# Kernel tuning notes

Measured on AMD Instinct MI355X. Metric: run time of the kernel, lower is better.

Reference implementation:

```python
import jax, jax.numpy as jnp
import numpy as np

N, E, F, H, C = 100000, 1600000, 64, 64, 40


def _agg_norm(row, col, mask, mtype, n):
    # A_tilde = A * mask (rows for 'target', cols for 'source'); fill_diag(A_tilde, 1.0)
    v = mask[row] if mtype == 'target' else mask[col]
    v = jnp.where(row == col, 0.0, v)  # diag entries replaced by fill_diag value 1
    deg = jax.ops.segment_sum(v, row, num_segments=n) + 1.0  # +1 from the filled diagonal
    d = jnp.where(deg > 0, jax.lax.rsqrt(deg), 0.0)  # D^-0.5, inf -> 0
    return d[row] * v * d[col], d * d  # off-diag edge values, diagonal values


def _spmm(row, col, vals, diag, x, n):
    # A_hat @ x with diagonal handled densely
    return jax.ops.segment_sum(vals[:, None] * x[col], row, num_segments=n) + diag[:, None] * x


def _sage(row, col, vals, diag, x, Wl, Wr, n):
    # SAGEConv(bias=False): lin_l(aggregate(A_hat, x)) + lin_r(x)
    return _spmm(row, col, vals, diag, x, n) @ Wl + x @ Wr


def setup_inputs() -> dict:
    key = jax.random.key(0)
    ks = jax.random.split(key, 16)
    g = lambda k, shape, s=0.1: jax.random.normal(k, shape, jnp.float32) * s
    return dict(
        x=g(ks[0], (N, F), 1.0),
        edge_index=jax.random.randint(ks[1], (2, E), 0, N),
        cc_mask=jax.random.randint(ks[2], (N,), 0, 2, dtype=jnp.int32),
        W1l=g(ks[3], (F, H)), W1r=g(ks[4], (F, H)),
        W2l=g(ks[5], (H, H)), W2r=g(ks[6], (H, H)),
        W3l=g(ks[7], (F, H)), W3r=g(ks[8], (F, H)),
        W4l=g(ks[9], (H, H)), W4r=g(ks[10], (H, H)),
        WX=g(ks[11], (F, H)),
        lam1=jnp.zeros((2,), jnp.float32),
        lam2=jnp.zeros((2,), jnp.float32),
        lin_W=g(ks[12], (H, C)),
        lin_b=jnp.zeros((C,), jnp.float32),
    )


def reference(x, edge_index, cc_mask, W1l, W1r, W2l, W2r, W3l, W3r, W4l, W4r, WX, lam1, lam2, lin_W, lin_b):
    n = x.shape[0]
    row, col = edge_index[1], edge_index[0]  # SparseTensor(row=ei[1], col=ei[0])
    cc = cc_mask.astype(x.dtype)
    rev = 1.0 - cc

    vl, dl = _agg_norm(row, col, cc, 'target', n)
    vll, dll = _agg_norm(row, col, cc, 'source', n)
    vh, dh = _agg_norm(row, col, rev, 'target', n)
    vhh, dhh = _agg_norm(row, col, rev, 'source', n)

    xl = jax.nn.relu(_sage(row, col, vl, dl, x, W1l, W1r, n))   # dropout = identity (eval)
    xl = _sage(row, col, vll, dll, xl, W2l, W2r, n)
    xh = jax.nn.relu(_sage(row, col, vh, dh, x, W3l, W3r, n))
    xh = _sage(row, col, vhh, dhh, xh, W4l, W4r, n)

    xm = x @ WX
    lamxl, laml = jax.nn.softmax(lam1)
    lamxh, lamh = jax.nn.softmax(lam2)
    lamx = lamxl * cc + lamxh * rev
    xf = jax.nn.relu(lamx[:, None] * xm + laml * xl + lamh * xh)
    return xf @ lin_W + lin_b
```

## Files before the change

### kernel.cpp

```cpp
#include <hip/hip_runtime.h>

#define PADF 68
#define RS_LOG 6
#define RSTRIDE 64


__global__ void k_deg(const int* __restrict__ ei, const int* __restrict__ cc,
                      unsigned long long* __restrict__ deg,
                      int* __restrict__ csr, int E, int H) {
    int t = blockIdx.x * blockDim.x + threadIdx.x;
    if (t >= H) return;
    int e0 = t, e1 = t + H;
    bool h1 = e1 < E;
    int c0 = ei[e0], r0 = ei[E + e0];
    int c1 = 0, r1 = 0;
    if (h1) { c1 = ei[e1]; r1 = ei[E + e1]; }
    bool a0 = (r0 != c0);
    bool a1 = h1 && (r1 != c1);
    int g0 = a0 ? (cc[c0] & 1) : 0;
    int g1 = a1 ? (cc[c1] & 1) : 0;
    unsigned long long old0 = 0, old1 = 0;
    if (a0) old0 = atomicAdd(&deg[r0], 0x100000000ULL + (unsigned long long)g0);
    if (a1) old1 = atomicAdd(&deg[r1], 0x100000000ULL + (unsigned long long)g1);
    if (a0) {
        int rk = (int)(old0 >> 32);
        if (rk < RSTRIDE)
            csr[(r0 << RS_LOG) + rk] = (int)((unsigned)c0 | ((unsigned)g0 << 31));
    }
    if (a1) {
        int rk = (int)(old1 >> 32);
        if (rk < RSTRIDE)
            csr[(r1 << RS_LOG) + rk] = (int)((unsigned)c1 | ((unsigned)g1 << 31));
    }
}

__global__ void k_dinv(const unsigned long long* __restrict__ deg,
                       const int* __restrict__ cc,
                       float* __restrict__ vs,
                       float* __restrict__ dll, float* __restrict__ dhh,
                       int* __restrict__ cnt, int n) {
    int i = blockIdx.x * blockDim.x + threadIdx.x;
    if (i >= n) return;
    unsigned long long d = deg[i];
    int c = (int)(d >> 32);
    int s = (int)(d & 0xffffffffULL);
    float fc = (float)c, fs = (float)s;
    float v = rsqrtf(fc + 1.0f);
    vs[i]  = cc[i] ? v : -v;
    dll[i] = rsqrtf(fs + 1.0f);
    dhh[i] = rsqrtf(fc - fs + 1.0f);
    cnt[i] = (c > RSTRIDE) ? RSTRIDE : c;
}


__device__ __forceinline__ void xreduce4(float4& a) {
    #pragma unroll
    for (int m = 16; m < 64; m <<= 1) {
        a.x += __shfl_xor(a.x, m, 64);
        a.y += __shfl_xor(a.y, m, 64);
        a.z += __shfl_xor(a.z, m, 64);
        a.w += __shfl_xor(a.w, m, 64);
    }
}

__device__ __forceinline__ void acc4(float4& a, float w, const float4& v) {
    a.x = fmaf(w, v.x, a.x); a.y = fmaf(w, v.y, a.y);
    a.z = fmaf(w, v.z, a.z); a.w = fmaf(w, v.w, a.w);
}

__device__ __forceinline__ void add4(float4& a, const float4& v) {
    a.x += v.x; a.y += v.y; a.z += v.z; a.w += v.w;
}

__global__ __launch_bounds__(256) void k_gather1(
        const int* __restrict__ cnt, const int* __restrict__ csr,
        const float* __restrict__ vs, const float* __restrict__ x,
        float* __restrict__ acc1, int n) {
    int w = (blockIdx.x * blockDim.x + threadIdx.x) >> 6;
    int lane = threadIdx.x & 63;
    if (w >= n) return;
    int r = w;
    int sub = lane >> 4, fe = lane & 15;
    int j0 = r << RS_LOG, j1 = j0 + cnt[r];
    float vsr = vs[r];
    bool ccr = vsr > 0.f;
    float4 a = make_float4(0.f, 0.f, 0.f, 0.f);
    int j = j0 + sub;
    for (; j + 4 < j1; j += 8) {
        unsigned e0 = (unsigned)csr[j], e1 = (unsigned)csr[j + 4];
        int c0 = (int)(e0 & 0x7fffffffu), c1 = (int)(e1 & 0x7fffffffu);
        bool f0 = (e0 >> 31) != 0, f1 = (e1 >> 31) != 0;
        float s0 = vs[c0], s1 = vs[c1];
        float w0 = (f0 == ccr) ? fabsf(s0) : 1.f;
        float w1 = (f1 == ccr) ? fabsf(s1) : 1.f;
        float4 v0 = *(const float4*)&x[(c0 << 6) + (fe << 2)];
        float4 v1 = *(const float4*)&x[(c1 << 6) + (fe << 2)];
        acc4(a, w0, v0);
        acc4(a, w1, v1);
    }
    if (j < j1) {
        unsigned e0 = (unsigned)csr[j];
        int c0 = (int)(e0 & 0x7fffffffu);
        bool f0 = (e0 >> 31) != 0;
        float s0 = vs[c0];
        float w0 = (f0 == ccr) ? fabsf(s0) : 1.f;
        float4 v0 = *(const float4*)&x[(c0 << 6) + (fe << 2)];
        acc4(a, w0, v0);
    }
    xreduce4(a);
    if (sub == 0) {
        float dr = fabsf(vsr);
        float4 o = make_float4(dr * a.x, dr * a.y, dr * a.z, dr * a.w);
        *(float4*)&acc1[(r << 6) + (fe << 2)] = o;
    }
}

__global__ __launch_bounds__(256) void k_gather2(
        const int* __restrict__ cnt, const int* __restrict__ csr,
        const float* __restrict__ XLs, const float* __restrict__ XHs,
        const float* __restrict__ dll, const float* __restrict__ dhh,
        float* __restrict__ accL, float* __restrict__ accH, int n) {
    int w = (blockIdx.x * blockDim.x + threadIdx.x) >> 6;
    int lane = threadIdx.x & 63;
    if (w >= n) return;
    int r = w;
    int sub = lane >> 4, fe = lane & 15;
    int j0 = r << RS_LOG, j1 = j0 + cnt[r];
    float4 aL = make_float4(0.f, 0.f, 0.f, 0.f);
    float4 aH = make_float4(0.f, 0.f, 0.f, 0.f);
    int j = j0 + sub;
    for (; j + 4 < j1; j += 8) {
        unsigned e0 = (unsigned)csr[j], e1 = (unsigned)csr[j + 4];
        int c0 = (int)(e0 & 0x7fffffffu), c1 = (int)(e1 & 0x7fffffffu);
        bool g0 = (e0 >> 31) != 0, g1 = (e1 >> 31) != 0;
        const float* p0 = g0 ? XLs : XHs;
        const float* p1 = g1 ? XLs : XHs;
        float4 v0 = *(const float4*)&p0[(c0 << 6) + (fe << 2)];
        float4 v1 = *(const float4*)&p1[(c1 << 6) + (fe << 2)];
        if (g0) add4(aL, v0); else add4(aH, v0);
        if (g1) add4(aL, v1); else add4(aH, v1);
    }
    if (j < j1) {
        unsigned e0 = (unsigned)csr[j];
        int c0 = (int)(e0 & 0x7fffffffu);
        bool g0 = (e0 >> 31) != 0;
        const float* p0 = g0 ? XLs : XHs;
        float4 v0 = *(const float4*)&p0[(c0 << 6) + (fe << 2)];
        if (g0) add4(aL, v0); else add4(aH, v0);
    }
    xreduce4(aL);
    xreduce4(aH);
    if (sub == 0) {
        float wl = dll[r], wh = dhh[r];
        float4 oL = make_float4(wl * aL.x, wl * aL.y, wl * aL.z, wl * aL.w);
        float4 oH = make_float4(wh * aH.x, wh * aH.y, wh * aH.z, wh * aH.w);
        *(float4*)&accL[(r << 6) + (fe << 2)] = oL;
        *(float4*)&accH[(r << 6) + (fe << 2)] = oH;
    }
}


__device__ __forceinline__ void fma4(float4& a, float s, const float4& b) {
    a.x = fmaf(s, b.x, a.x);
    a.y = fmaf(s, b.y, a.y);
    a.z = fmaf(s, b.z, a.z);
    a.w = fmaf(s, b.w, a.w);
}

__device__ __forceinline__ void gemm16(const float* __restrict__ sA,
                                       const float* __restrict__ sB,
                                       int mq, int fq, float4 (&acc)[4]) {
    #pragma unroll 2
    for (int k4 = 0; k4 < 16; ++k4) {
        float4 b0 = *(const float4*)&sB[(k4 * 4 + 0) * 64 + fq * 4];
        float4 b1 = *(const float4*)&sB[(k4 * 4 + 1) * 64 + fq * 4];
        float4 b2 = *(const float4*)&sB[(k4 * 4 + 2) * 64 + fq * 4];
        float4 b3 = *(const float4*)&sB[(k4 * 4 + 3) * 64 + fq * 4];
        #pragma unroll
        for (int r = 0; r < 4; ++r) {
            float4 a = *(const float4*)&sA[(mq * 4 + r) * PADF + k4 * 4];
            fma4(acc[r], a.x, b0);
            fma4(acc[r], a.y, b1);
            fma4(acc[r], a.z, b2);
            fma4(acc[r], a.w, b3);
        }
    }
}

__device__ __forceinline__ void zero4(float4 (&acc)[4]) {
    #pragma unroll
    for (int r = 0; r < 4; ++r) acc[r] = make_float4(0.f, 0.f, 0.f, 0.f);
}

__device__ __forceinline__ void stageB(const float* __restrict__ W, float* sB, int tid) {
    const float4* w4 = (const float4*)W;
    float4* s4 = (float4*)sB;
    #pragma unroll
    for (int p = 0; p < 4; ++p) s4[p * 256 + tid] = w4[p * 256 + tid];
}

__device__ __forceinline__ void stageBsum(const float* __restrict__ Wa,
                                          const float* __restrict__ Wb,
                                          float* sB, int tid) {
    const float4* a4 = (const float4*)Wa;
    const float4* b4 = (const float4*)Wb;
    float4* s4 = (float4*)sB;
    #pragma unroll
    for (int p = 0; p < 4; ++p) {
        float4 a = a4[p * 256 + tid], b = b4[p * 256 + tid];
        s4[p * 256 + tid] = make_float4(a.x + b.x, a.y + b.y, a.z + b.z, a.w + b.w);
    }
}

__global__ __launch_bounds__(256) void k_dense1(
        const float* __restrict__ x, const float* __restrict__ acc1,
        const float* __restrict__ vs,
        const float* __restrict__ dll, const float* __restrict__ dhh,
        const float* __restrict__ W1l, const float* __restrict__ W1r,
        const float* __restrict__ W3l, const float* __restrict__ W3r,
        float* __restrict__ XLs, float* __restrict__ XHs, int n) {
    __shared__ float sX[64 * PADF];
    __shared__ float sG[64 * PADF];
    __shared__ float sB[64 * 64];
    __shared__ float sGl[64];
    __shared__ float sSL[64];
    __shared__ float sSH[64];
    __shared__ float sDs[64];
    int tid = threadIdx.x, b = blockIdx.x;
    int mq = tid >> 4, fq = tid & 15;
    if (tid < 64) {
        int i = b * 64 + tid;
        float v = (i < n) ? vs[i] : 1.f;
        sDs[tid] = v * v;
        sGl[tid] = (v > 0.f) ? 1.f : 0.f;
        sSL[tid] = (i < n) ? dll[i] : 0.f;
        sSH[tid] = (i < n) ? dhh[i] : 0.f;
    }
    __syncthreads();
    const float4* x4 = (const float4*)x;
    const float4* a4g = (const float4*)acc1;
    int lim4 = n * 16;
    #pragma unroll
    for (int p = 0; p < 4; ++p) {
        int idx = p * 256 + tid;
        int m = idx >> 4, c4 = idx & 15;
        int g = b * 1024 + idx;
        float4 vx = make_float4(0.f, 0.f, 0.f, 0.f), va = vx;
        if (g < lim4) { vx = x4[g]; va = a4g[g]; }
        float dm1 = sDs[m] - 1.f;
        *(float4*)&sX[m * PADF + c4 * 4] = vx;
        *(float4*)&sG[m * PADF + c4 * 4] = make_float4(
            fmaf(dm1, vx.x, va.x), fmaf(dm1, vx.y, va.y),
            fmaf(dm1, vx.z, va.z), fmaf(dm1, vx.w, va.w));
    }
    stageBsum(W1l, W1r, sB, tid);
    __syncthreads();
    float4 accT[4], accP[4];
    zero4(accT);
    gemm16(sX, sB, mq, fq, accT);
    __syncthreads();
    stageB(W1l, sB, tid);
    __syncthreads();
    zero4(accP);
    gemm16(sG, sB, mq, fq, accP);
    #pragma unroll
    for (int r = 0; r < 4; ++r) {
        int i = b * 64 + mq * 4 + r;
        if (i < n) {
            float gl = sGl[mq * 4 + r];
            float sc = sSL[mq * 4 + r];
            float4 o;
            o.x = sc * fmaxf(fmaf(gl, accP[r].x, accT[r].x), 0.f);
            o.y = sc * fmaxf(fmaf(gl, accP[r].y, accT[r].y), 0.f);
            o.z = sc * fmaxf(fmaf(gl, accP[r].z, accT[r].z), 0.f);
            o.w = sc * fmaxf(fmaf(gl, accP[r].w, accT[r].w), 0.f);
            *(float4*)&XLs[(i << 6) + fq * 4] = o;
        }
    }
    __syncthreads();
    stageBsum(W3l, W3r, sB, tid);
    __syncthreads();
    zero4(accT);
    gemm16(sX, sB, mq, fq, accT);
    __syncthreads();
    stageB(W3l, sB, tid);
    __syncthreads();
    zero4(accP);
    gemm16(sG, sB, mq, fq, accP);
    #pragma unroll
    for (int r = 0; r < 4; ++r) {
        int i = b * 64 + mq * 4 + r;
        if (i < n) {
            float gh = 1.f - sGl[mq * 4 + r];
            float sc = sSH[mq * 4 + r];
            float4 o;
            o.x = sc * fmaxf(fmaf(gh, accP[r].x, accT[r].x), 0.f);
            o.y = sc * fmaxf(fmaf(gh, accP[r].y, accT[r].y), 0.f);
            o.z = sc * fmaxf(fmaf(gh, accP[r].z, accT[r].z), 0.f);
            o.w = sc * fmaxf(fmaf(gh, accP[r].w, accT[r].w), 0.f);
            *(float4*)&XHs[(i << 6) + fq * 4] = o;
        }
    }
}

__global__ __launch_bounds__(256) void k_dense2ch(
        const float* __restrict__ Xcs, float* __restrict__ accC,
        const float* __restrict__ dd,
        const float* __restrict__ Wl, const float* __restrict__ Wr,
        const float* __restrict__ lam, int n) {
    __shared__ float sXc[64 * PADF];
    __shared__ float sA2[64 * PADF];
    __shared__ float sB[64 * 64];
    __shared__ float sD[64];
    __shared__ float sI[64];
    int tid = threadIdx.x, b = blockIdx.x;
    int mq = tid >> 4, fq = tid & 15;
    if (tid < 64) {
        int i = b * 64 + tid;
        float a = (i < n) ? dd[i] : 1.f;
        sD[tid] = a;
        sI[tid] = 1.f / a;
    }
    __syncthreads();
    const float4* x4 = (const float4*)Xcs;
    const float4* a4g = (const float4*)accC;
    int lim4 = n * 16;
    #pragma unroll
    for (int p = 0; p < 4; ++p) {
        int idx = p * 256 + tid;
        int m = idx >> 4, c4 = idx & 15;
        int g = b * 1024 + idx;
        float4 vx = make_float4(0.f, 0.f, 0.f, 0.f), va = vx;
        if (g < lim4) { vx = x4[g]; va = a4g[g]; }
        float ds = sD[m], iv = sI[m];
        *(float4*)&sXc[m * PADF + c4 * 4] = make_float4(iv * vx.x, iv * vx.y,
                                                        iv * vx.z, iv * vx.w);
        *(float4*)&sA2[m * PADF + c4 * 4] = make_float4(
            fmaf(ds, vx.x, va.x), fmaf(ds, vx.y, va.y),
            fmaf(ds, vx.z, va.z), fmaf(ds, vx.w, va.w));
    }
    stageB(Wl, sB, tid);
    __syncthreads();
    float4 accP[4], accT[4];
    zero4(accP);
    gemm16(sA2, sB, mq, fq, accP);
    __syncthreads();
    stageB(Wr, sB, tid);
    __syncthreads();
    zero4(accT);
    gemm16(sXc, sB, mq, fq, accT);
    float e0 = __expf(lam[0]), e1 = __expf(lam[1]);
    float scale = e1 / (e0 + e1);
    #pragma unroll
    for (int r = 0; r < 4; ++r) {
        int i = b * 64 + mq * 4 + r;
        if (i < n) {
            float4 o;
            o.x = scale * (accP[r].x + accT[r].x);
            o.y = scale * (accP[r].y + accT[r].y);
            o.z = scale * (accP[r].z + accT[r].z);
            o.w = scale * (accP[r].w + accT[r].w);
            *(float4*)&accC[(i << 6) + fq * 4] = o;
        }
    }
}

__global__ __launch_bounds__(256) void k_dense2b(
        const float* __restrict__ x,
        const float* __restrict__ tmpL, const float* __restrict__ tmpH,
        const float* __restrict__ vs,
        const float* __restrict__ WX,
        const float* __restrict__ lam1, const float* __restrict__ lam2,
        const float* __restrict__ linW, const float* __restrict__ linb,
        float* __restrict__ out, int n, int C) {
    __shared__ float sXA[64 * PADF];
    __shared__ float sB[64 * 64];
    __shared__ float sLx[64];
    int tid = threadIdx.x, b = blockIdx.x;
    int mq = tid >> 4, fq = tid & 15;
    float e0 = __expf(lam1[0]), e1 = __expf(lam1[1]);
    float lamxl = e0 / (e0 + e1);
    float g0 = __expf(lam2[0]), g1 = __expf(lam2[1]);
    float lamxh = g0 / (g0 + g1);
    if (tid < 64) {
        int i = b * 64 + tid;
        bool c = (i < n) ? (vs[i] > 0.f) : false;
        sLx[tid] = c ? lamxl : lamxh;
    }
    const float4* x4 = (const float4*)x;
    int lim4 = n * 16;
    #pragma unroll
    for (int p = 0; p < 4; ++p) {
        int idx = p * 256 + tid;
        int m = idx >> 4, c4 = idx & 15;
        int g = b * 1024 + idx;
        float4 vx = make_float4(0.f, 0.f, 0.f, 0.f);
        if (g < lim4) vx = x4[g];
        *(float4*)&sXA[m * PADF + c4 * 4] = vx;
    }
    stageB(WX, sB, tid);
    __syncthreads();
    float4 accT[4];
    zero4(accT);
    gemm16(sXA, sB, mq, fq, accT);
    float4 xf[4];
    #pragma unroll
    for (int r = 0; r < 4; ++r) {
        int i = b * 64 + mq * 4 + r;
        float lamx = sLx[mq * 4 + r];
        float4 tl = make_float4(0.f, 0.f, 0.f, 0.f), th = tl;
        if (i < n) {
            tl = *(const float4*)&tmpL[(i << 6) + fq * 4];
            th = *(const float4*)&tmpH[(i << 6) + fq * 4];
        }
        xf[r].x = fmaxf(fmaf(lamx, accT[r].x, tl.x + th.x), 0.f);
        xf[r].y = fmaxf(fmaf(lamx, accT[r].y, tl.y + th.y), 0.f);
        xf[r].z = fmaxf(fmaf(lamx, accT[r].z, tl.z + th.z), 0.f);
        xf[r].w = fmaxf(fmaf(lamx, accT[r].w, tl.w + th.w), 0.f);
    }
    __syncthreads();
    #pragma unroll
    for (int r = 0; r < 4; ++r)
        *(float4*)&sXA[(mq * 4 + r) * PADF + fq * 4] = xf[r];
    #pragma unroll
    for (int p = 0; p < 16; ++p) {
        int idx = p * 256 + tid;
        int k = idx >> 6, c = idx & 63;
        sB[idx] = (c < C) ? linW[k * C + c] : 0.f;
    }
    __syncthreads();
    float4 accO[4];
    zero4(accO);
    gemm16(sXA, sB, mq, fq, accO);
    if (fq * 4 + 3 < C) {
        #pragma unroll
        for (int r = 0; r < 4; ++r) {
            int i = b * 64 + mq * 4 + r;
            if (i < n) {
                float4 o;
                o.x = accO[r].x + linb[fq * 4 + 0];
                o.y = accO[r].y + linb[fq * 4 + 1];
                o.z = accO[r].z + linb[fq * 4 + 2];
                o.w = accO[r].w + linb[fq * 4 + 3];
                *(float4*)&out[i * C + fq * 4] = o;
            }
        }
    }
}


extern "C" void kernel_launch(void* const* d_in, const int* in_sizes, int n_in,
                              void* d_out, int out_size, void* d_ws, size_t ws_size,
                              hipStream_t stream) {
    const float* x    = (const float*)d_in[0];
    const int*   ei   = (const int*)d_in[1];
    const int*   cc   = (const int*)d_in[2];
    const float* W1l  = (const float*)d_in[3];
    const float* W1r  = (const float*)d_in[4];
    const float* W2l  = (const float*)d_in[5];
    const float* W2r  = (const float*)d_in[6];
    const float* W3l  = (const float*)d_in[7];
    const float* W3r  = (const float*)d_in[8];
    const float* W4l  = (const float*)d_in[9];
    const float* W4r  = (const float*)d_in[10];
    const float* WX   = (const float*)d_in[11];
    const float* lam1 = (const float*)d_in[12];
    const float* lam2 = (const float*)d_in[13];
    const float* linW = (const float*)d_in[14];
    const float* linb = (const float*)d_in[15];

    int n = in_sizes[2];
    int E = in_sizes[1] / 2;
    int C = in_sizes[15];

    char* ws = (char*)d_ws;
    size_t nf = (size_t)n * 64 * sizeof(float);
    float* bufA = (float*)ws; ws += nf;
    float* bufB = (float*)ws; ws += nf;
    float* XLb  = (float*)ws; ws += nf;
    float* XHb  = (float*)ws; ws += nf;
    float* vsb  = (float*)ws; ws += (size_t)n * sizeof(float);
    float* dll  = (float*)ws; ws += (size_t)n * sizeof(float);
    float* dhh  = (float*)ws; ws += (size_t)n * sizeof(float);
    int*   cnt  = (int*)ws;   ws += (size_t)n * sizeof(int);
    unsigned long long* deg = (unsigned long long*)ws; ws += (size_t)n * sizeof(unsigned long long);
    int* csr = (int*)ws; ws += (size_t)n * RSTRIDE * sizeof(int);

    hipMemsetAsync(deg, 0, (size_t)n * sizeof(unsigned long long), stream);

    int H = (E + 1) / 2;
    k_deg<<<(H + 255) / 256, 256, 0, stream>>>(ei, cc, deg, csr, E, H);
    k_dinv<<<(n + 255) / 256, 256, 0, stream>>>(deg, cc, vsb, dll, dhh, cnt, n);

    int gatherBlocks = (n + 3) / 4;
    int nb = (n + 63) / 64;
    k_gather1<<<gatherBlocks, 256, 0, stream>>>(cnt, csr, vsb, x, bufA, n);
    k_dense1<<<nb, 256, 0, stream>>>(x, bufA, vsb, dll, dhh,
                                     W1l, W1r, W3l, W3r, XLb, XHb, n);
    k_gather2<<<gatherBlocks, 256, 0, stream>>>(cnt, csr, XLb, XHb,
                                                dll, dhh, bufA, bufB, n);
    k_dense2ch<<<nb, 256, 0, stream>>>(XLb, bufA, dll, W2l, W2r, lam1, n);
    k_dense2ch<<<nb, 256, 0, stream>>>(XHb, bufB, dhh, W4l, W4r, lam2, n);
    k_dense2b<<<nb, 256, 0, stream>>>(x, bufA, bufB, vsb, WX, lam1, lam2, linW, linb,
                                      (float*)d_out, n, C);
}
```

Measured before the change: 483.1 us.

## Overlap degree/CSR build with degree-independent GEMMs and merge dense2 kernels

Merges the edge-atomic degree/CSR construction and the three degree-independent dense products (x@(W1l+W1r), x@(W3l+W3r), x@WX) into one launch, so the matmuls fill the GPU while the atomics run. k_dense1 then reads these precomputed partials instead of recomputing them. The two dense2ch launches and dense2b are fused into a single k_dense2, which removes the round trip of the per-channel temporaries through global memory. In exchange it adds extra n×64 buffers that are written and reread, and k_pre's block-index branching may make scheduling between the atomic and GEMM parts uneven.

```diff
diff --git a/kernel.cpp b/kernel.cpp
--- a/kernel.cpp
+++ b/kernel.cpp
@@ -5,32 +5,116 @@
 #define RSTRIDE 64
 
 
-__global__ void k_deg(const int* __restrict__ ei, const int* __restrict__ cc,
-                      unsigned long long* __restrict__ deg,
-                      int* __restrict__ csr, int E, int H) {
-    int t = blockIdx.x * blockDim.x + threadIdx.x;
-    if (t >= H) return;
-    int e0 = t, e1 = t + H;
-    bool h1 = e1 < E;
-    int c0 = ei[e0], r0 = ei[E + e0];
-    int c1 = 0, r1 = 0;
-    if (h1) { c1 = ei[e1]; r1 = ei[E + e1]; }
-    bool a0 = (r0 != c0);
-    bool a1 = h1 && (r1 != c1);
-    int g0 = a0 ? (cc[c0] & 1) : 0;
-    int g1 = a1 ? (cc[c1] & 1) : 0;
-    unsigned long long old0 = 0, old1 = 0;
-    if (a0) old0 = atomicAdd(&deg[r0], 0x100000000ULL + (unsigned long long)g0);
-    if (a1) old1 = atomicAdd(&deg[r1], 0x100000000ULL + (unsigned long long)g1);
-    if (a0) {
-        int rk = (int)(old0 >> 32);
-        if (rk < RSTRIDE)
-            csr[(r0 << RS_LOG) + rk] = (int)((unsigned)c0 | ((unsigned)g0 << 31));
-    }
-    if (a1) {
-        int rk = (int)(old1 >> 32);
-        if (rk < RSTRIDE)
-            csr[(r1 << RS_LOG) + rk] = (int)((unsigned)c1 | ((unsigned)g1 << 31));
+__device__ __forceinline__ void fma4(float4& a, float s, const float4& b) {
+    a.x = fmaf(s, b.x, a.x);
+    a.y = fmaf(s, b.y, a.y);
+    a.z = fmaf(s, b.z, a.z);
+    a.w = fmaf(s, b.w, a.w);
+}
+
+__device__ __forceinline__ void gemm16(const float* __restrict__ sA,
+                                       const float* __restrict__ sB,
+                                       int mq, int fq, float4 (&acc)[4]) {
+    #pragma unroll 2
+    for (int k4 = 0; k4 < 16; ++k4) {
+        float4 b0 = *(const float4*)&sB[(k4 * 4 + 0) * 64 + fq * 4];
+        float4 b1 = *(const float4*)&sB[(k4 * 4 + 1) * 64 + fq * 4];
+        float4 b2 = *(const float4*)&sB[(k4 * 4 + 2) * 64 + fq * 4];
+        float4 b3 = *(const float4*)&sB[(k4 * 4 + 3) * 64 + fq * 4];
+        #pragma unroll
+        for (int r = 0; r < 4; ++r) {
+            float4 a = *(const float4*)&sA[(mq * 4 + r) * PADF + k4 * 4];
+            fma4(acc[r], a.x, b0);
+            fma4(acc[r], a.y, b1);
+            fma4(acc[r], a.z, b2);
+            fma4(acc[r], a.w, b3);
+        }
+    }
+}
+
+__device__ __forceinline__ void zero4(float4 (&acc)[4]) {
+    #pragma unroll
+    for (int r = 0; r < 4; ++r) acc[r] = make_float4(0.f, 0.f, 0.f, 0.f);
+}
+
+__device__ __forceinline__ void stageB(const float* __restrict__ W, float* sB, int tid) {
+    const float4* w4 = (const float4*)W;
+    float4* s4 = (float4*)sB;
+    #pragma unroll
+    for (int p = 0; p < 4; ++p) s4[p * 256 + tid] = w4[p * 256 + tid];
+}
+
+__device__ __forceinline__ void stageBsum(const float* __restrict__ Wa,
+                                          const float* __restrict__ Wb,
+                                          float* sB, int tid) {
+    const float4* a4 = (const float4*)Wa;
+    const float4* b4 = (const float4*)Wb;
+    float4* s4 = (float4*)sB;
+    #pragma unroll
+    for (int p = 0; p < 4; ++p) {
+        float4 a = a4[p * 256 + tid], b = b4[p * 256 + tid];
+        s4[p * 256 + tid] = make_float4(a.x + b.x, a.y + b.y, a.z + b.z, a.w + b.w);
+    }
+}
+
+
+__global__ __launch_bounds__(256) void k_pre(
+        const int* __restrict__ ei, const int* __restrict__ cc,
+        const float* __restrict__ x,
+        const float* __restrict__ W1l, const float* __restrict__ W1r,
+        const float* __restrict__ W3l, const float* __restrict__ W3r,
+        const float* __restrict__ WX,
+        unsigned long long* __restrict__ deg, int* __restrict__ csr,
+        float* __restrict__ XL0, float* __restrict__ XH0, float* __restrict__ XM,
+        int E, int Q, int EB, int nb, int n) {
+    __shared__ float sX[64 * PADF];
+    __shared__ float sB[64 * 64];
+    int bid = blockIdx.x, tid = threadIdx.x;
+    if (bid < EB) {
+        int t = bid * 256 + tid;
+        if (t < Q) {
+            #pragma unroll
+            for (int k = 0; k < 4; ++k) {
+                int e = t + k * Q;
+                if (e >= E) break;
+                int c = ei[e], r = ei[E + e];
+                if (r == c) continue;
+                int g = cc[c] & 1;
+                unsigned long long old =
+                    atomicAdd(&deg[r], 0x100000000ULL + (unsigned long long)g);
+                int rk = (int)(old >> 32);
+                if (rk < RSTRIDE)
+                    csr[(r << RS_LOG) + rk] = (int)((unsigned)c | ((unsigned)g << 31));
+            }
+        }
+        return;
+    }
+    int q = bid - EB;
+    int ms = q / nb, tb = q - ms * nb;
+    int mq = tid >> 4, fq = tid & 15;
+    const float4* x4 = (const float4*)x;
+    int lim4 = n * 16;
+    #pragma unroll
+    for (int p = 0; p < 4; ++p) {
+        int idx = p * 256 + tid;
+        int m = idx >> 4, c4 = idx & 15;
+        int g = tb * 1024 + idx;
+        float4 vx = make_float4(0.f, 0.f, 0.f, 0.f);
+        if (g < lim4) vx = x4[g];
+        *(float4*)&sX[m * PADF + c4 * 4] = vx;
+    }
+    if (ms == 0)      stageBsum(W1l, W1r, sB, tid);
+    else if (ms == 1) stageBsum(W3l, W3r, sB, tid);
+    else              stageB(WX, sB, tid);
+    __syncthreads();
+    float4 acc[4];
+    zero4(acc);
+    gemm16(sX, sB, mq, fq, acc);
+    float* OUT = (ms == 0) ? XL0 : ((ms == 1) ? XH0 : XM);
+    #pragma unroll
+    for (int r = 0; r < 4; ++r) {
+        int i = tb * 64 + mq * 4 + r;
+        if (i < n) *(float4*)&OUT[(i << 6) + fq * 4] = acc[r];
     }
 }
 
@@ -159,67 +243,13 @@
     }
 }
 
-
-__device__ __forceinline__ void fma4(float4& a, float s, const float4& b) {
-    a.x = fmaf(s, b.x, a.x);
-    a.y = fmaf(s, b.y, a.y);
-    a.z = fmaf(s, b.z, a.z);
-    a.w = fmaf(s, b.w, a.w);
-}
-
-__device__ __forceinline__ void gemm16(const float* __restrict__ sA,
-                                       const float* __restrict__ sB,
-                                       int mq, int fq, float4 (&acc)[4]) {
-    #pragma unroll 2
-    for (int k4 = 0; k4 < 16; ++k4) {
-        float4 b0 = *(const float4*)&sB[(k4 * 4 + 0) * 64 + fq * 4];
-        float4 b1 = *(const float4*)&sB[(k4 * 4 + 1) * 64 + fq * 4];
-        float4 b2 = *(const float4*)&sB[(k4 * 4 + 2) * 64 + fq * 4];
-        float4 b3 = *(const float4*)&sB[(k4 * 4 + 3) * 64 + fq * 4];
-        #pragma unroll
-        for (int r = 0; r < 4; ++r) {
-            float4 a = *(const float4*)&sA[(mq * 4 + r) * PADF + k4 * 4];
-            fma4(acc[r], a.x, b0);
-            fma4(acc[r], a.y, b1);
-            fma4(acc[r], a.z, b2);
-            fma4(acc[r], a.w, b3);
-        }
-    }
-}
-
-__device__ __forceinline__ void zero4(float4 (&acc)[4]) {
-    #pragma unroll
-    for (int r = 0; r < 4; ++r) acc[r] = make_float4(0.f, 0.f, 0.f, 0.f);
-}
-
-__device__ __forceinline__ void stageB(const float* __restrict__ W, float* sB, int tid) {
-    const float4* w4 = (const float4*)W;
-    float4* s4 = (float4*)sB;
-    #pragma unroll
-    for (int p = 0; p < 4; ++p) s4[p * 256 + tid] = w4[p * 256 + tid];
-}
-
-__device__ __forceinline__ void stageBsum(const float* __restrict__ Wa,
-                                          const float* __restrict__ Wb,
-                                          float* sB, int tid) {
-    const float4* a4 = (const float4*)Wa;
-    const float4* b4 = (const float4*)Wb;
-    float4* s4 = (float4*)sB;
-    #pragma unroll
-    for (int p = 0; p < 4; ++p) {
-        float4 a = a4[p * 256 + tid], b = b4[p * 256 + tid];
-        s4[p * 256 + tid] = make_float4(a.x + b.x, a.y + b.y, a.z + b.z, a.w + b.w);
-    }
-}
-
 __global__ __launch_bounds__(256) void k_dense1(
         const float* __restrict__ x, const float* __restrict__ acc1,
         const float* __restrict__ vs,
         const float* __restrict__ dll, const float* __restrict__ dhh,
-        const float* __restrict__ W1l, const float* __restrict__ W1r,
-        const float* __restrict__ W3l, const float* __restrict__ W3r,
+        const float* __restrict__ W1l, const float* __restrict__ W3l,
+        const float* __restrict__ XL0, const float* __restrict__ XH0,
         float* __restrict__ XLs, float* __restrict__ XHs, int n) {
-    __shared__ float sX[64 * PADF];
     __shared__ float sG[64 * PADF];
     __shared__ float sB[64 * 64];
     __shared__ float sGl[64];
@@ -248,180 +278,159 @@
         float4 vx = make_float4(0.f, 0.f, 0.f, 0.f), va = vx;
         if (g < lim4) { vx = x4[g]; va = a4g[g]; }
         float dm1 = sDs[m] - 1.f;
-        *(float4*)&sX[m * PADF + c4 * 4] = vx;
         *(float4*)&sG[m * PADF + c4 * 4] = make_float4(
             fmaf(dm1, vx.x, va.x), fmaf(dm1, vx.y, va.y),
             fmaf(dm1, vx.z, va.z), fmaf(dm1, vx.w, va.w));
     }
-    stageBsum(W1l, W1r, sB, tid);
-    __syncthreads();
-    float4 accT[4], accP[4];
-    zero4(accT);
-    gemm16(sX, sB, mq, fq, accT);
-    __syncthreads();
     stageB(W1l, sB, tid);
     __syncthreads();
+    float4 accP[4], accQ[4];
     zero4(accP);
     gemm16(sG, sB, mq, fq, accP);
+    __syncthreads();
+    stageB(W3l, sB, tid);
+    __syncthreads();
+    zero4(accQ);
+    gemm16(sG, sB, mq, fq, accQ);
     #pragma unroll
     for (int r = 0; r < 4; ++r) {
         int i = b * 64 + mq * 4 + r;
         if (i < n) {
-            float gl = sGl[mq * 4 + r];
-            float sc = sSL[mq * 4 + r];
-            float4 o;
-            o.x = sc * fmaxf(fmaf(gl, accP[r].x, accT[r].x), 0.f);
-            o.y = sc * fmaxf(fmaf(gl, accP[r].y, accT[r].y), 0.f);
-            o.z = sc * fmaxf(fmaf(gl, accP[r].z, accT[r].z), 0.f);
-            o.w = sc * fmaxf(fmaf(gl, accP[r].w, accT[r].w), 0.f);
-            *(float4*)&XLs[(i << 6) + fq * 4] = o;
+            int jj = mq * 4 + r;
+            float gl = sGl[jj], gh = 1.f - gl;
+            float scl = sSL[jj], sch = sSH[jj];
+            float4 t0 = *(const float4*)&XL0[(i << 6) + fq * 4];
+            float4 t1 = *(const float4*)&XH0[(i << 6) + fq * 4];
+            float4 oL, oH;
+            oL.x = scl * fmaxf(fmaf(gl, accP[r].x, t0.x), 0.f);
+            oL.y = scl * fmaxf(fmaf(gl, accP[r].y, t0.y), 0.f);
+            oL.z = scl * fmaxf(fmaf(gl, accP[r].z, t0.z), 0.f);
+            oL.w = scl * fmaxf(fmaf(gl, accP[r].w, t0.w), 0.f);
+            oH.x = sch * fmaxf(fmaf(gh, accQ[r].x, t1.x), 0.f);
+            oH.y = sch * fmaxf(fmaf(gh, accQ[r].y, t1.y), 0.f);
+            oH.z = sch * fmaxf(fmaf(gh, accQ[r].z, t1.z), 0.f);
+            oH.w = sch * fmaxf(fmaf(gh, accQ[r].w, t1.w), 0.f);
+            *(float4*)&XLs[(i << 6) + fq * 4] = oL;
+            *(float4*)&XHs[(i << 6) + fq * 4] = oH;
         }
     }
-    __syncthreads();
-    stageBsum(W3l, W3r, sB, tid);
-    __syncthreads();
-    zero4(accT);
-    gemm16(sX, sB, mq, fq, accT);
-    __syncthreads();
-    stageB(W3l, sB, tid);
-    __syncthreads();
-    zero4(accP);
-    gemm16(sG, sB, mq, fq, accP);
-    #pragma unroll
-    for (int r = 0; r < 4; ++r) {
-        int i = b * 64 + mq * 4 + r;
-        if (i < n) {
-            float gh = 1.f - sGl[mq * 4 + r];
-            float sc = sSH[mq * 4 + r];
-            float4 o;
-            o.x = sc * fmaxf(fmaf(gh, accP[r].x, accT[r].x), 0.f);
-            o.y = sc * fmaxf(fmaf(gh, accP[r].y, accT[r].y), 0.f);
-            o.z = sc * fmaxf(fmaf(gh, accP[r].z, accT[r].z), 0.f);
-            o.w = sc * fmaxf(fmaf(gh, accP[r].w, accT[r].w), 0.f);
-            *(float4*)&XHs[(i << 6) + fq * 4] = o;
-        }
-    }
-}
-
-__global__ __launch_bounds__(256) void k_dense2ch(
-        const float* __restrict__ Xcs, float* __restrict__ accC,
-        const float* __restrict__ dd,
-        const float* __restrict__ Wl, const float* __restrict__ Wr,
-        const float* __restrict__ lam, int n) {
+}
+
+__global__ __launch_bounds__(256) void k_dense2(
+        const float* __restrict__ XLs, const float* __restrict__ accL,
+        const float* __restrict__ XHs, const float* __restrict__ accH,
+        const float* __restrict__ XM, const float* __restrict__ vs,
+        const float* __restrict__ dll, const float* __restrict__ dhh,
+        const float* __restrict__ W2l, const float* __restrict__ W2r,
+        const float* __restrict__ W4l, const float* __restrict__ W4r,
+        const float* __restrict__ lam1, const float* __restrict__ lam2,
+        const float* __restrict__ linW, const float* __restrict__ linb,
+        float* __restrict__ out, int n, int C) {
     __shared__ float sXc[64 * PADF];
     __shared__ float sA2[64 * PADF];
     __shared__ float sB[64 * 64];
-    __shared__ float sD[64];
-    __shared__ float sI[64];
+    __shared__ float sDl[64], sIl[64], sDh[64], sIh[64], sLx[64];
     int tid = threadIdx.x, b = blockIdx.x;
     int mq = tid >> 4, fq = tid & 15;
+    float e0 = __expf(lam1[0]), e1 = __expf(lam1[1]);
+    float lamxl = e0 / (e0 + e1), laml = e1 / (e0 + e1);
+    float g0 = __expf(lam2[0]), g1 = __expf(lam2[1]);
+    float lamxh = g0 / (g0 + g1), lamh = g1 / (g0 + g1);
     if (tid < 64) {
         int i = b * 64 + tid;
-        float a = (i < n) ? dd[i] : 1.f;
-        sD[tid] = a;
-        sI[tid] = 1.f / a;
-    }
-    __syncthreads();
-    const float4* x4 = (const float4*)Xcs;
-    const float4* a4g = (const float4*)accC;
+        float a = (i < n) ? dll[i] : 1.f;
+        float h = (i < n) ? dhh[i] : 1.f;
+        sDl[tid] = a; sIl[tid] = 1.f / a;
+        sDh[tid] = h; sIh[tid] = 1.f / h;
+        bool c = (i < n) ? (vs[i] > 0.f) : false;
+        sLx[tid] = c ? lamxl : lamxh;
+    }
+    __syncthreads();
     int lim4 = n * 16;
-    #pragma unroll
-    for (int p = 0; p < 4; ++p) {
-        int idx = p * 256 + tid;
-        int m = idx >> 4, c4 = idx & 15;
-        int g = b * 1024 + idx;
-        float4 vx = make_float4(0.f, 0.f, 0.f, 0.f), va = vx;
-        if (g < lim4) { vx = x4[g]; va = a4g[g]; }
-        float ds = sD[m], iv = sI[m];
-        *(float4*)&sXc[m * PADF + c4 * 4] = make_float4(iv * vx.x, iv * vx.y,
-                                                        iv * vx.z, iv * vx.w);
-        *(float4*)&sA2[m * PADF + c4 * 4] = make_float4(
-            fmaf(ds, vx.x, va.x), fmaf(ds, vx.y, va.y),
-            fmaf(ds, vx.z, va.z), fmaf(ds, vx.w, va.w));
-    }
-    stageB(Wl, sB, tid);
+    {
+        const float4* x4 = (const float4*)XLs;
+        const float4* a4g = (const float4*)accL;
+        #pragma unroll
+        for (int p = 0; p < 4; ++p) {
+            int idx = p * 256 + tid;
+            int m = idx >> 4, c4 = idx & 15;
+            int g = b * 1024 + idx;
+            float4 vx = make_float4(0.f, 0.f, 0.f, 0.f), va = vx;
+            if (g < lim4) { vx = x4[g]; va = a4g[g]; }
+            float ds = sDl[m], iv = sIl[m];
+            *(float4*)&sXc[m * PADF + c4 * 4] = make_float4(iv * vx.x, iv * vx.y,
+                                                            iv * vx.z, iv * vx.w);
+            *(float4*)&sA2[m * PADF + c4 * 4] = make_float4(
+                fmaf(ds, vx.x, va.x), fmaf(ds, vx.y, va.y),
+                fmaf(ds, vx.z, va.z), fmaf(ds, vx.w, va.w));
+        }
+        stageB(W2l, sB, tid);
+    }
     __syncthreads();
     float4 accP[4], accT[4];
     zero4(accP);
     gemm16(sA2, sB, mq, fq, accP);
     __syncthreads();
-    stageB(Wr, sB, tid);
+    stageB(W2r, sB, tid);
     __syncthreads();
     zero4(accT);
     gemm16(sXc, sB, mq, fq, accT);
-    float e0 = __expf(lam[0]), e1 = __expf(lam[1]);
-    float scale = e1 / (e0 + e1);
+    float4 tmpL[4];
     #pragma unroll
     for (int r = 0; r < 4; ++r) {
-        int i = b * 64 + mq * 4 + r;
-        if (i < n) {
-            float4 o;
-            o.x = scale * (accP[r].x + accT[r].x);
-            o.y = scale * (accP[r].y + accT[r].y);
-            o.z = scale * (accP[r].z + accT[r].z);
-            o.w = scale * (accP[r].w + accT[r].w);
-            *(float4*)&accC[(i << 6) + fq * 4] = o;
+        tmpL[r].x = laml * (accP[r].x + accT[r].x);
+        tmpL[r].y = laml * (accP[r].y + accT[r].y);
+        tmpL[r].z = laml * (accP[r].z + accT[r].z);
+        tmpL[r].w = laml * (accP[r].w + accT[r].w);
+    }
+    __syncthreads();
+    {
+        const float4* x4 = (const float4*)XHs;
+        const float4* a4g = (const float4*)accH;
+        #pragma unroll
+        for (int p = 0; p < 4; ++p) {
+            int idx = p * 256 + tid;
+            int m = idx >> 4, c4 = idx & 15;
+            int g = b * 1024 + idx;
+            float4 vx = make_float4(0.f, 0.f, 0.f, 0.f), va = vx;
+            if (g < lim4) { vx = x4[g]; va = a4g[g]; }
+            float ds = sDh[m], iv = sIh[m];
+            *(float4*)&sXc[m * PADF + c4 * 4] = make_float4(iv * vx.x, iv * vx.y,
+                                                            iv * vx.z, iv * vx.w);
+            *(float4*)&sA2[m * PADF + c4 * 4] = make_float4(
+                fmaf(ds, vx.x, va.x), fmaf(ds, vx.y, va.y),
+                fmaf(ds, vx.z, va.z), fmaf(ds, vx.w, va.w));
         }
-    }
-}
-
-__global__ __launch_bounds__(256) void k_dense2b(
-        const float* __restrict__ x,
-        const float* __restrict__ tmpL, const float* __restrict__ tmpH,
-        const float* __restrict__ vs,
-        const float* __restrict__ WX,
-        const float* __restrict__ lam1, const float* __restrict__ lam2,
-        const float* __restrict__ linW, const float* __restrict__ linb,
-        float* __restrict__ out, int n, int C) {
-    __shared__ float sXA[64 * PADF];
-    __shared__ float sB[64 * 64];
-    __shared__ float sLx[64];
-    int tid = threadIdx.x, b = blockIdx.x;
-    int mq = tid >> 4, fq = tid & 15;
-    float e0 = __expf(lam1[0]), e1 = __expf(lam1[1]);
-    float lamxl = e0 / (e0 + e1);
-    float g0 = __expf(lam2[0]), g1 = __expf(lam2[1]);
-    float lamxh = g0 / (g0 + g1);
-    if (tid < 64) {
-        int i = b * 64 + tid;
-        bool c = (i < n) ? (vs[i] > 0.f) : false;
-        sLx[tid] = c ? lamxl : lamxh;
-    }
-    const float4* x4 = (const float4*)x;
-    int lim4 = n * 16;
-    #pragma unroll
-    for (int p = 0; p < 4; ++p) {
-        int idx = p * 256 + tid;
-        int m = idx >> 4, c4 = idx & 15;
-        int g = b * 1024 + idx;
-        float4 vx = make_float4(0.f, 0.f, 0.f, 0.f);
-        if (g < lim4) vx = x4[g];
-        *(float4*)&sXA[m * PADF + c4 * 4] = vx;
-    }
-    stageB(WX, sB, tid);
-    __syncthreads();
-    float4 accT[4];
+        stageB(W4l, sB, tid);
+    }
+    __syncthreads();
+    zero4(accP);
+    gemm16(sA2, sB, mq, fq, accP);
+    __syncthreads();
+    stageB(W4r, sB, tid);
+    __syncthreads();
     zero4(accT);
-    gemm16(sXA, sB, mq, fq, accT);
+    gemm16(sXc, sB, mq, fq, accT);
     float4 xf[4];
     #pragma unroll
     for (int r = 0; r < 4; ++r) {
         int i = b * 64 + mq * 4 + r;
         float lamx = sLx[mq * 4 + r];
-        float4 tl = make_float4(0.f, 0.f, 0.f, 0.f), th = tl;
-        if (i < n) {
-            tl = *(const float4*)&tmpL[(i << 6) + fq * 4];
-            th = *(const float4*)&tmpH[(i << 6) + fq * 4];
-        }
-        xf[r].x = fmaxf(fmaf(lamx, accT[r].x, tl.x + th.x), 0.f);
-        xf[r].y = fmaxf(fmaf(lamx, accT[r].y, tl.y + th.y), 0.f);
-        xf[r].z = fmaxf(fmaf(lamx, accT[r].z, tl.z + th.z), 0.f);
-        xf[r].w = fmaxf(fmaf(lamx, accT[r].w, tl.w + th.w), 0.f);
+        float4 xm = make_float4(0.f, 0.f, 0.f, 0.f);
+        if (i < n) xm = *(const float4*)&XM[(i << 6) + fq * 4];
+        float th_x = lamh * (accP[r].x + accT[r].x);
+        float th_y = lamh * (accP[r].y + accT[r].y);
+        float th_z = lamh * (accP[r].z + accT[r].z);
+        float th_w = lamh * (accP[r].w + accT[r].w);
+        xf[r].x = fmaxf(fmaf(lamx, xm.x, tmpL[r].x + th_x), 0.f);
+        xf[r].y = fmaxf(fmaf(lamx, xm.y, tmpL[r].y + th_y), 0.f);
+        xf[r].z = fmaxf(fmaf(lamx, xm.z, tmpL[r].z + th_z), 0.f);
+        xf[r].w = fmaxf(fmaf(lamx, xm.w, tmpL[r].w + th_w), 0.f);
     }
     __syncthreads();
     #pragma unroll
     for (int r = 0; r < 4; ++r)
-        *(float4*)&sXA[(mq * 4 + r) * PADF + fq * 4] = xf[r];
+        *(float4*)&sA2[(mq * 4 + r) * PADF + fq * 4] = xf[r];
     #pragma unroll
     for (int p = 0; p < 16; ++p) {
         int idx = p * 256 + tid;
@@ -431,7 +440,7 @@
     __syncthreads();
     float4 accO[4];
     zero4(accO);
-    gemm16(sXA, sB, mq, fq, accO);
+    gemm16(sA2, sB, mq, fq, accO);
     if (fq * 4 + 3 < C) {
         #pragma unroll
         for (int r = 0; r < 4; ++r) {
@@ -476,7 +485,9 @@
     char* ws = (char*)d_ws;
     size_t nf = (size_t)n * 64 * sizeof(float);
     float* bufA = (float*)ws; ws += nf;
-    float* bufB = (float*)ws; ws += nf;
+    float* bufC = (float*)ws; ws += nf;
+    float* XH0  = (float*)ws; ws += nf;
+    float* XMb  = (float*)ws; ws += nf;
     float* XLb  = (float*)ws; ws += nf;
     float* XHb  = (float*)ws; ws += nf;
     float* vsb  = (float*)ws; ws += (size_t)n * sizeof(float);
@@ -488,19 +499,21 @@
 
     hipMemsetAsync(deg, 0, (size_t)n * sizeof(unsigned long long), stream);
 
-    int H = (E + 1) / 2;
-    k_deg<<<(H + 255) / 256, 256, 0, stream>>>(ei, cc, deg, csr, E, H);
+    int Q = (E + 3) / 4;
+    int EB = (Q + 255) / 256;
+    int nb = (n + 63) / 64;
+    k_pre<<<EB + 3 * nb, 256, 0, stream>>>(ei, cc, x, W1l, W1r, W3l, W3r, WX,
+                                           deg, csr, bufC, XH0, XMb,
+                                           E, Q, EB, nb, n);
     k_dinv<<<(n + 255) / 256, 256, 0, stream>>>(deg, cc, vsb, dll, dhh, cnt, n);
 
     int gatherBlocks = (n + 3) / 4;
-    int nb = (n + 63) / 64;
     k_gather1<<<gatherBlocks, 256, 0, stream>>>(cnt, csr, vsb, x, bufA, n);
-    k_dense1<<<nb, 256, 0, stream>>>(x, bufA, vsb, dll, dhh,
-                                     W1l, W1r, W3l, W3r, XLb, XHb, n);
+    k_dense1<<<nb, 256, 0, stream>>>(x, bufA, vsb, dll, dhh, W1l, W3l,
+                                     bufC, XH0, XLb, XHb, n);
     k_gather2<<<gatherBlocks, 256, 0, stream>>>(cnt, csr, XLb, XHb,
-                                                dll, dhh, bufA, bufB, n);
-    k_dense2ch<<<nb, 256, 0, stream>>>(XLb, bufA, dll, W2l, W2r, lam1, n);
-    k_dense2ch<<<nb, 256, 0, stream>>>(XHb, bufB, dhh, W4l, W4r, lam2, n);
-    k_dense2b<<<nb, 256, 0, stream>>>(x, bufA, bufB, vsb, WX, lam1, lam2, linW, linb,
-                                      (float*)d_out, n, C);
-}
+                                                dll, dhh, bufA, bufC, n);
+    k_dense2<<<nb, 256, 0, stream>>>(XLb, bufA, XHb, bufC, XMb, vsb, dll, dhh,
+                                     W2l, W2r, W4l, W4r, lam1, lam2, linW, linb,
+                                     (float*)d_out, n, C);
+}
```

Result: faster. 458.6 us (-5.1%).
